# Kernel tuning notes

Hardware: AMD Instinct MI355X
Metric: run time of the kernel (lower is better)

Reference implementation:

```python
import jax, jax.numpy as jnp
import numpy as np

B, L, E, H = 1, 2048, 1024, 16
HW = E // H  # head width = 64
SCALE = HW ** -0.5


def setup_inputs() -> dict:
    key = jax.random.key(0)
    ks = jax.random.split(key, 8)
    x = jax.random.normal(ks[0], (B, L, E), dtype=jnp.float32)
    mask = jax.random.bernoulli(ks[1], 0.9, (B, L))
    mask = mask.at[:, 0].set(True)  # guarantee at least one valid key per batch
    bias = jax.random.normal(ks[2], (B, L, L, H), dtype=jnp.float32)
    # torch nn.Linear stores weight as [out, in]; we keep that convention
    w_proj = jax.random.normal(ks[3], (3 * E, E), dtype=jnp.float32) * (E ** -0.5)
    w_o = jax.random.normal(ks[4], (E, E), dtype=jnp.float32) * (E ** -0.5)
    b_o = jax.random.normal(ks[5], (E,), dtype=jnp.float32) * 0.02
    w_g = jax.random.normal(ks[6], (E, E), dtype=jnp.float32) * (E ** -0.5)
    b_g = jax.random.normal(ks[7], (E,), dtype=jnp.float32) * 0.02
    return {"x": x, "mask": mask, "bias": bias, "w_proj": w_proj,
            "w_o": w_o, "b_o": b_o, "w_g": w_g, "b_g": b_g}


def reference(x, mask, bias, w_proj, w_o, b_o, w_g, b_g):
    # proj -> [B, L, 3E], rearrange '(h c)' with h=H so each head slice holds [q|k|v]
    t = jnp.einsum('ble,fe->blf', x, w_proj)               # [B, L, 3E]
    t = t.reshape(B, L, H, 3 * HW).transpose(0, 2, 1, 3)   # [B, H, L, 3*HW]
    q, k, v = jnp.split(t, 3, axis=-1)                     # each [B, H, L, HW]
    a = jnp.einsum('bhqc,bhkc->bhqk', SCALE * q, k)        # [B, H, L, L]
    a = a + bias.transpose(0, 3, 1, 2)                     # bias: [B,Lq,Lk,H] -> [B,H,Lq,Lk]
    a = jnp.where(mask[:, None, None, :], a, -jnp.inf)
    a = jax.nn.softmax(a, axis=-1)
    y = jnp.einsum('bhqk,bhkc->bqhc', a, v).reshape(B, L, E)
    g = jax.nn.sigmoid(jnp.einsum('ble,fe->blf', x, w_g) + b_g)
    y = g * y
    return jnp.einsum('ble,fe->blf', y, w_o) + b_o
```

## Files before the change

kernel.cpp:

```cpp
#include <hip/hip_runtime.h>
#include <stdint.h>

#define LSEQ 2048
#define EMB  1024
#define NH   16
#define HWID 64
#define SCALEF 0.125f

typedef __attribute__((ext_vector_type(4))) float  f32x4;
typedef __attribute__((ext_vector_type(8))) short  bf16x8;
typedef __attribute__((ext_vector_type(8))) unsigned short u16x8;
typedef __attribute__((ext_vector_type(4))) unsigned short u16x4;

static __device__ __forceinline__ unsigned short f2bf(float f) {
    union { float f; unsigned int u; } v; v.f = f;
    unsigned int r = (v.u + 0x7FFFu + ((v.u >> 16) & 1u)) >> 16;
    return (unsigned short)r;
}
static __device__ __forceinline__ float bf2f(unsigned short h) {
    union { unsigned int u; float f; } v; v.u = ((unsigned int)h) << 16;
    return v.f;
}

static __device__ __forceinline__ void gload_lds16(const void* g, void* l) {
    __builtin_amdgcn_global_load_lds((const __attribute__((address_space(1))) void*)g,
                                     (__attribute__((address_space(3))) void*)l,
                                     16, 0, 0);
}

__global__ __launch_bounds__(256) void convert_kernel(
    const float* __restrict__ x, const float* __restrict__ wp,
    const float* __restrict__ wg, const float* __restrict__ wo,
    unsigned short* __restrict__ xb, unsigned short* __restrict__ wcat,
    unsigned short* __restrict__ wob)
{
    const int NX  = (LSEQ * EMB) / 4;
    const int NWP = (3 * EMB * EMB) / 4;
    const int NWG = (EMB * EMB) / 4;
    const int NWO = (EMB * EMB) / 4;
    const int total = NX + NWP + NWG + NWO;
    for (int i = blockIdx.x * blockDim.x + threadIdx.x; i < total;
         i += gridDim.x * blockDim.x) {
        const float4* src; unsigned short* dst; int j;
        if (i < NX)                  { src = (const float4*)x;  dst = xb;                  j = i; }
        else if (i < NX + NWP)       { src = (const float4*)wp; dst = wcat;                j = i - NX; }
        else if (i < NX + NWP + NWG) { src = (const float4*)wg; dst = wcat + 3 * EMB * EMB; j = i - NX - NWP; }
        else                         { src = (const float4*)wo; dst = wob;                 j = i - NX - NWP - NWG; }
        float4 v = src[j];
        u16x4 o;
        o.x = f2bf(v.x); o.y = f2bf(v.y); o.z = f2bf(v.z); o.w = f2bf(v.w);
        *(u16x4*)(dst + (size_t)j * 4) = o;
    }
}

__global__ void decode_mask_kernel(const unsigned char* __restrict__ mask,
                                   float* __restrict__ mbias)
{
    __shared__ int cnt;
    if (threadIdx.x == 0) cnt = 0;
    __syncthreads();
    int c = 0;
    for (int i = threadIdx.x; i < LSEQ; i += 256) c += (mask[i] != 0);
    atomicAdd(&cnt, c);
    __syncthreads();
    bool isbyte = cnt > LSEQ / 2;
    for (int k = threadIdx.x; k < LSEQ; k += 256) {
        bool v;
        if (isbyte) v = (mask[k] != 0);
        else        v = ((mask[4*k] | mask[4*k+1] | mask[4*k+2] | mask[4*k+3]) != 0);
        mbias[k] = v ? 0.f : -1e30f;
    }
}

#define BM 128
#define BN 128
#define BK 64

__global__ __launch_bounds__(256) void gemm_bt_kernel(
    const unsigned short* __restrict__ A, const unsigned short* __restrict__ B,
    void* __restrict__ Cout, const float* __restrict__ biasN,
    int M, int N, int K, int epi)
{
    __shared__ unsigned short As[BM][BK];
    __shared__ unsigned short Bs[BN][BK];
    const int tid  = threadIdx.x;
    const int lane = tid & 63;
    const int w    = tid >> 6;
    const int wr   = w >> 1, wc = w & 1;
    const int row0 = blockIdx.y * BM;
    const int col0 = blockIdx.x * BN;
    const int lr = lane & 15;
    const int lg = lane >> 4;

    f32x4 acc[4][4];
    const f32x4 zf = {0.f, 0.f, 0.f, 0.f};
#pragma unroll
    for (int m = 0; m < 4; ++m)
#pragma unroll
        for (int n = 0; n < 4; ++n) acc[m][n] = zf;

    const char* Ab = (const char*)(A + (size_t)row0 * K);
    const char* Bb = (const char*)(B + (size_t)col0 * K);
    const int Kb = K * 2;

    for (int kt = 0; kt < K; kt += BK) {
#pragma unroll
        for (int i = 0; i < 4; ++i) {
            int o = (i * 256 + tid) * 16;
            int r = o >> 7, cb = o & 127;
            gload_lds16(Ab + (size_t)r * Kb + kt * 2 + cb, (char*)As + o);
        }
#pragma unroll
        for (int i = 0; i < 4; ++i) {
            int o = (i * 256 + tid) * 16;
            int r = o >> 7, cb = o & 127;
            gload_lds16(Bb + (size_t)r * Kb + kt * 2 + cb, (char*)Bs + o);
        }
        __syncthreads();
#pragma unroll
        for (int kk = 0; kk < 2; ++kk) {
            bf16x8 af[4], bfr[4];
            const int lk = kk * 32 + lg * 8;
#pragma unroll
            for (int m = 0; m < 4; ++m) af[m]  = *(const bf16x8*)&As[wr * 64 + m * 16 + lr][lk];
#pragma unroll
            for (int n = 0; n < 4; ++n) bfr[n] = *(const bf16x8*)&Bs[wc * 64 + n * 16 + lr][lk];
#pragma unroll
            for (int m = 0; m < 4; ++m)
#pragma unroll
                for (int n = 0; n < 4; ++n)
                    acc[m][n] = __builtin_amdgcn_mfma_f32_16x16x32_bf16(af[m], bfr[n], acc[m][n], 0, 0, 0);
        }
        __syncthreads();
    }

#pragma unroll
    for (int m = 0; m < 4; ++m)
#pragma unroll
        for (int n = 0; n < 4; ++n) {
            const int col = col0 + wc * 64 + n * 16 + lr;
#pragma unroll
            for (int r = 0; r < 4; ++r) {
                const int row = row0 + wr * 64 + m * 16 + lg * 4 + r;
                if (epi == 0)
                    ((unsigned short*)Cout)[(size_t)row * N + col] = f2bf(acc[m][n][r]);
                else
                    ((float*)Cout)[(size_t)row * N + col] = acc[m][n][r] + biasN[col];
            }
        }
}

__global__ __launch_bounds__(256) void rearrange_kernel(
    const unsigned short* __restrict__ T, const float* __restrict__ bg,
    unsigned short* __restrict__ Qh, unsigned short* __restrict__ Kh,
    unsigned short* __restrict__ G)
{
    const int l = blockIdx.x;
    const int t = threadIdx.x;
    const unsigned short* trow = T + (size_t)l * 4096;
    {
        const int tt = t & 127;
        const int h  = tt >> 3;
        const int c0 = (tt & 7) * 8;
        const bool isq = (t < 128);
        const int srcoff = h * 192 + (isq ? 0 : 64) + c0;
        u16x8 v = *(const u16x8*)(trow + srcoff);
        if (isq) {
#pragma unroll
            for (int j = 0; j < 8; ++j) v[j] = f2bf(bf2f(v[j]) * SCALEF);
        }
        unsigned short* dst = (isq ? Qh : Kh) + ((size_t)h * LSEQ + l) * HWID + c0;
        *(u16x8*)dst = v;
    }
    {
        const int f0 = t * 4;
        float4 b4 = *(const float4*)(bg + f0);
        u16x4 tv = *(const u16x4*)(trow + 3 * EMB + f0);
        u16x4 o;
        o.x = f2bf(1.f / (1.f + __expf(-(bf2f(tv.x) + b4.x))));
        o.y = f2bf(1.f / (1.f + __expf(-(bf2f(tv.y) + b4.y))));
        o.z = f2bf(1.f / (1.f + __expf(-(bf2f(tv.z) + b4.z))));
        o.w = f2bf(1.f / (1.f + __expf(-(bf2f(tv.w) + b4.w))));
        *(u16x4*)(G + (size_t)l * EMB + f0) = o;
    }
}

__global__ __launch_bounds__(256) void vtrans_kernel(
    const unsigned short* __restrict__ T, unsigned short* __restrict__ VT)
{
    __shared__ unsigned short tile[64][72];
    const int h  = blockIdx.x & 15;
    const int lt = blockIdx.x >> 4;
    const int l0 = lt * 64;
    const int t  = threadIdx.x;
    {
        const int i = t >> 2, c0 = (t & 3) * 16;
        const unsigned short* src = T + (size_t)(l0 + i) * 4096 + h * 192 + 128;
        *(u16x8*)&tile[i][c0]     = *(const u16x8*)(src + c0);
        *(u16x8*)&tile[i][c0 + 8] = *(const u16x8*)(src + c0 + 8);
    }
    __syncthreads();
    {
        const int c = t >> 2, j0 = (t & 3) * 16;
        unsigned short* dst = VT + ((size_t)h * HWID + c) * LSEQ + l0 + j0;
        u16x8 a, b;
#pragma unroll
        for (int j = 0; j < 8; ++j) a[j] = tile[j0 + j][c];
#pragma unroll
        for (int j = 0; j < 8; ++j) b[j] = tile[j0 + 8 + j][c];
        *(u16x8*)dst       = a;
        *(u16x8*)(dst + 8) = b;
    }
}

#define NT 32

__global__ __launch_bounds__(1024) void attn_kernel(
    const unsigned short* __restrict__ Qh, const unsigned short* __restrict__ Kh,
    const unsigned short* __restrict__ VT, const float* __restrict__ bias,
    const float* __restrict__ mbias,
    float* __restrict__ Op, float* __restrict__ Ml)
{
    __shared__ float bias_s[2][16][576];
    __shared__ unsigned short ps[16][16][40];
    __shared__ float mk[1024];

    const int tid  = threadIdx.x;
    const int lane = tid & 63;
    const int w    = tid >> 6;
    const int qsub = blockIdx.x >> 1;
    const int sp   = blockIdx.x & 1;
    const int h    = w;
    const int q0   = qsub * 16;
    const int koff = sp * 1024;
    const int lr   = lane & 15;
    const int lg   = lane >> 4;

    const unsigned short* Qbase = Qh + ((size_t)h * LSEQ + q0) * HWID;
    const bf16x8 qa0 = *(const bf16x8*)(Qbase + lr * HWID + lg * 8);
    const bf16x8 qa1 = *(const bf16x8*)(Qbase + lr * HWID + 32 + lg * 8);

    const unsigned short* Kbase = Kh + ((size_t)h * LSEQ + koff) * HWID;
    const unsigned short* Vbase = VT + (size_t)h * HWID * LSEQ + koff;

    const int li   = tid >> 1;
    const int bq   = li >> 5;
    const int bk   = li & 31;
    const int half = tid & 1;
    const float* bsrc0 = bias +
        ((size_t)(q0 + bq) * LSEQ + (koff + bk)) * NH + half * 8;
    const int bidx = bq * 36 + bk;

    auto loadBias = [&](int t, float4* bv) {
        const float* src = bsrc0 + (size_t)t * 32 * NH;
        bv[0] = *(const float4*)(src);
        bv[1] = *(const float4*)(src + 4);
    };
    auto writeBias = [&](int slot, const float4* bv) {
#pragma unroll
        for (int j = 0; j < 4; ++j) {
            bias_s[slot][half * 8 + j][bidx]     = ((const float*)&bv[0])[j];
            bias_s[slot][half * 8 + 4 + j][bidx] = ((const float*)&bv[1])[j];
        }
    };
    auto loadK = [&](int t, bf16x8 (&kb)[2][2]) {
        const int kgl = t * 32;
#pragma unroll
        for (int t2 = 0; t2 < 2; ++t2) {
            const unsigned short* kp = Kbase + (size_t)(kgl + t2 * 16 + lr) * HWID + lg * 8;
            kb[t2][0] = *(const bf16x8*)kp;
            kb[t2][1] = *(const bf16x8*)(kp + 32);
        }
    };

    bf16x8 ones;
#pragma unroll
    for (int j2 = 0; j2 < 8; ++j2) ones[j2] = (short)0x3F80;

    float mrow[4];
    f32x4 acc[4], lsum;
    const f32x4 zf = {0.f, 0.f, 0.f, 0.f};
#pragma unroll
    for (int r = 0; r < 4; ++r) mrow[r] = -1e30f;
#pragma unroll
    for (int c = 0; c < 4; ++c) acc[c] = zf;
    lsum = zf;

    float4 bv[2];
    bf16x8 kbA[2][2], kbB[2][2];
    loadBias(0, bv);
    loadK(0, kbA);
    mk[tid] = mbias[koff + tid];
    __syncthreads();
    writeBias(0, bv);
    asm volatile("s_waitcnt lgkmcnt(0)" ::: "memory");
    __builtin_amdgcn_s_barrier();

    const unsigned short (*psb)[40] = nullptr; (void)psb;

    auto body = [&](int t, bf16x8 (&kbCur)[2][2], bf16x8 (&kbNxt)[2][2]) {
        const int kgl = t * 32;

        bf16x8 vb[4];
#pragma unroll
        for (int ct = 0; ct < 4; ++ct)
            vb[ct] = *(const bf16x8*)(Vbase + (size_t)(ct * 16 + lr) * LSEQ + kgl + lg * 8);
        asm volatile("" ::: "memory");
        if (t + 1 < NT) loadK(t + 1, kbNxt);
        asm volatile("" ::: "memory");
        if (t + 1 < NT) loadBias(t + 1, bv);
        asm volatile("" ::: "memory");

        f32x4 S[2];
#pragma unroll
        for (int t2 = 0; t2 < 2; ++t2) {
            f32x4 s = zf;
            s = __builtin_amdgcn_mfma_f32_16x16x32_bf16(qa0, kbCur[t2][0], s, 0, 0, 0);
            s = __builtin_amdgcn_mfma_f32_16x16x32_bf16(qa1, kbCur[t2][1], s, 0, 0, 0);
            S[t2] = s;
        }

        const float* bpl = &bias_s[t & 1][w][0];
        const float m0 = mk[kgl + lr];
        const float m1 = mk[kgl + 16 + lr];
        float sc0[4], sc1[4], lm[4];
#pragma unroll
        for (int r = 0; r < 4; ++r) {
            const int qrow = (lg * 4 + r) * 36;
            sc0[r] = S[0][r] + bpl[qrow + lr] + m0;
            sc1[r] = S[1][r] + bpl[qrow + 16 + lr] + m1;
            lm[r] = fmaxf(sc0[r], sc1[r]);
        }
        const float need = fmaxf(fmaxf(lm[0] - mrow[0], lm[1] - mrow[1]),
                                 fmaxf(lm[2] - mrow[2], lm[3] - mrow[3]));
        if (!__all(need <= 8.0f)) {
            float rm[4];
#pragma unroll
            for (int r = 0; r < 4; ++r) rm[r] = lm[r];
#pragma unroll
            for (int off = 1; off < 16; off <<= 1)
#pragma unroll
                for (int r = 0; r < 4; ++r)
                    rm[r] = fmaxf(rm[r], __shfl_xor(rm[r], off, 64));
            float sf[4];
#pragma unroll
            for (int r = 0; r < 4; ++r) {
                const float mn = fmaxf(mrow[r], rm[r]);
                sf[r] = __expf(mrow[r] - mn);
                mrow[r] = mn;
            }
#pragma unroll
            for (int ct = 0; ct < 4; ++ct)
#pragma unroll
                for (int r = 0; r < 4; ++r) acc[ct][r] *= sf[r];
#pragma unroll
            for (int r = 0; r < 4; ++r) lsum[r] *= sf[r];
        }

        float p0[4], p1[4];
#pragma unroll
        for (int r = 0; r < 4; ++r) {
            p0[r] = __expf(sc0[r] - mrow[r]);
            p1[r] = __expf(sc1[r] - mrow[r]);
        }

#pragma unroll
        for (int r = 0; r < 4; ++r) {
            ps[w][lg * 4 + r][lr]      = f2bf(p0[r]);
            ps[w][lg * 4 + r][16 + lr] = f2bf(p1[r]);
        }
        const bf16x8 pa = *(const bf16x8*)&ps[w][lr][lg * 8];

#pragma unroll
        for (int ct = 0; ct < 4; ++ct)
            acc[ct] = __builtin_amdgcn_mfma_f32_16x16x32_bf16(pa, vb[ct], acc[ct], 0, 0, 0);
        lsum = __builtin_amdgcn_mfma_f32_16x16x32_bf16(pa, ones, lsum, 0, 0, 0);

        if (t + 1 < NT) writeBias((t + 1) & 1, bv);
        asm volatile("s_waitcnt lgkmcnt(0)" ::: "memory");
        __builtin_amdgcn_s_barrier();
    };

#pragma unroll 1
    for (int tt = 0; tt < NT; tt += 2) {
        body(tt,     kbA, kbB);
        body(tt + 1, kbB, kbA);
    }

    const size_t rowb = ((size_t)sp * NH + h) * LSEQ;
#pragma unroll
    for (int ct = 0; ct < 4; ++ct)
#pragma unroll
        for (int r = 0; r < 4; ++r) {
            const int q = q0 + lg * 4 + r;
            Op[(rowb + q) * HWID + ct * 16 + lr] = acc[ct][r];
        }
    if (lr == 0) {
#pragma unroll
        for (int r = 0; r < 4; ++r) {
            const int q = q0 + lg * 4 + r;
            Ml[(rowb + q) * 2 + 0] = mrow[r];
            Ml[(rowb + q) * 2 + 1] = lsum[r];
        }
    }
}

__global__ __launch_bounds__(256) void combine_kernel(
    const float* __restrict__ Op, const float* __restrict__ Ml,
    const unsigned short* __restrict__ G, unsigned short* __restrict__ Yb)
{
    const int t   = threadIdx.x;
    const int c   = t & 63;
    const int row = blockIdx.x * 4 + (t >> 6);
    const int h   = row >> 11;
    const int q   = row & (LSEQ - 1);
    const size_t r0 = (size_t)h * LSEQ + q;
    const size_t r1 = ((size_t)NH + h) * LSEQ + q;
    const float m0 = Ml[r0 * 2 + 0], l0 = Ml[r0 * 2 + 1];
    const float m1 = Ml[r1 * 2 + 0], l1 = Ml[r1 * 2 + 1];
    const float mx = fmaxf(m0, m1);
    const float a0 = __expf(m0 - mx), a1 = __expf(m1 - mx);
    const float inv = 1.f / (l0 * a0 + l1 * a1);
    const float o0 = Op[r0 * HWID + c];
    const float o1 = Op[r1 * HWID + c];
    const float y = (o0 * a0 + o1 * a1) * inv;
    const int e = h * HWID + c;
    const float g = bf2f(G[(size_t)q * EMB + e]);
    Yb[(size_t)q * EMB + e] = f2bf(y * g);
}

extern "C" void kernel_launch(void* const* d_in, const int* in_sizes, int n_in,
                              void* d_out, int out_size, void* d_ws, size_t ws_size,
                              hipStream_t stream) {
    const float*         x      = (const float*)d_in[0];
    const unsigned char* mask   = (const unsigned char*)d_in[1];
    const float*         bias   = (const float*)d_in[2];
    const float*         w_proj = (const float*)d_in[3];
    const float*         w_o    = (const float*)d_in[4];
    const float*         b_o    = (const float*)d_in[5];
    const float*         w_g    = (const float*)d_in[6];
    const float*         b_g    = (const float*)d_in[7];
    float* out = (float*)d_out;
    (void)in_sizes; (void)n_in; (void)out_size; (void)ws_size;

    char* p = (char*)d_ws;
    auto alloc = [&](size_t bytes) {
        char* r = p; p += (bytes + 255) & ~(size_t)255; return r;
    };
    unsigned short* xb    = (unsigned short*)alloc((size_t)LSEQ * EMB * 2);
    unsigned short* wcat  = (unsigned short*)alloc((size_t)4 * EMB * EMB * 2);
    unsigned short* wob   = (unsigned short*)alloc((size_t)EMB * EMB * 2);
    unsigned short* T     = (unsigned short*)alloc((size_t)LSEQ * 4096 * 2);
    unsigned short* Qh    = (unsigned short*)alloc((size_t)NH * LSEQ * HWID * 2);
    unsigned short* Kh    = (unsigned short*)alloc((size_t)NH * LSEQ * HWID * 2);
    unsigned short* VT    = (unsigned short*)alloc((size_t)NH * HWID * LSEQ * 2);
    unsigned short* G     = (unsigned short*)alloc((size_t)LSEQ * EMB * 2);
    unsigned short* Yb    = (unsigned short*)alloc((size_t)LSEQ * EMB * 2);
    float*          mb    = (float*)alloc((size_t)LSEQ * 4);
    float*          Op    = (float*)alloc((size_t)2 * NH * LSEQ * HWID * 4);
    float*          Ml    = (float*)alloc((size_t)2 * NH * LSEQ * 2 * 4);

    convert_kernel<<<1024, 256, 0, stream>>>(x, w_proj, w_g, w_o, xb, wcat, wob);
    decode_mask_kernel<<<1, 256, 0, stream>>>(mask, mb);
    gemm_bt_kernel<<<dim3(4096 / BN, LSEQ / BM), 256, 0, stream>>>(
        xb, wcat, (void*)T, nullptr, LSEQ, 4096, EMB, 0);
    rearrange_kernel<<<LSEQ, 256, 0, stream>>>(T, b_g, Qh, Kh, G);
    vtrans_kernel<<<NH * (LSEQ / 64), 256, 0, stream>>>(T, VT);
    attn_kernel<<<256, 1024, 0, stream>>>(Qh, Kh, VT, bias, mb, Op, Ml);
    combine_kernel<<<NH * LSEQ / 4, 256, 0, stream>>>(Op, Ml, G, Yb);
    gemm_bt_kernel<<<dim3(EMB / BN, LSEQ / BM), 256, 0, stream>>>(
        Yb, wob, (void*)out, b_o, LSEQ, EMB, EMB, 1);
}
```

Baseline: 238.0 us.

## Deepen bias prefetch to two tiles ahead with explicit vmcnt waits

Bias loads are now issued two tiles ahead and held in ping-pong register buffers, and K stays one tile ahead. Indices are clamped so the loop no longer needs tail conditionals. Explicit sched_barriers and partial s_waitcnt vmcnt counts replace the compiler's conservative waits, so the MFMA work can start while later global loads are still in flight. In exchange it uses more registers and depends on hand-counted vmcnt values matching the load order the compiler emits. The final iterations also issue redundant clamped loads.

```diff
diff --git a/kernel.cpp b/kernel.cpp
--- a/kernel.cpp
+++ b/kernel.cpp
@@ -252,7 +252,8 @@
     const int bidx = bq * 36 + bk;
 
     auto loadBias = [&](int t, float4* bv) {
-        const float* src = bsrc0 + (size_t)t * 32 * NH;
+        const int tc = (t < NT) ? t : NT - 1;
+        const float* src = bsrc0 + (size_t)tc * 32 * NH;
         bv[0] = *(const float4*)(src);
         bv[1] = *(const float4*)(src + 4);
     };
@@ -264,7 +265,8 @@
         }
     };
     auto loadK = [&](int t, bf16x8 (&kb)[2][2]) {
-        const int kgl = t * 32;
+        const int tc = (t < NT) ? t : NT - 1;
+        const int kgl = tc * 32;
 #pragma unroll
         for (int t2 = 0; t2 < 2; ++t2) {
             const unsigned short* kp = Kbase + (size_t)(kgl + t2 * 16 + lr) * HWID + lg * 8;
@@ -286,31 +288,33 @@
     for (int c = 0; c < 4; ++c) acc[c] = zf;
     lsum = zf;
 
-    float4 bv[2];
+    float4 tmp[2], bvA[2], bvB[2];
     bf16x8 kbA[2][2], kbB[2][2];
-    loadBias(0, bv);
+    loadBias(0, tmp);
+    loadBias(1, bvA);
     loadK(0, kbA);
     mk[tid] = mbias[koff + tid];
     __syncthreads();
-    writeBias(0, bv);
+    writeBias(0, tmp);
     asm volatile("s_waitcnt lgkmcnt(0)" ::: "memory");
     __builtin_amdgcn_s_barrier();
 
-    const unsigned short (*psb)[40] = nullptr; (void)psb;
-
-    auto body = [&](int t, bf16x8 (&kbCur)[2][2], bf16x8 (&kbNxt)[2][2]) {
+    auto body = [&](int t, bf16x8 (&kbCur)[2][2], bf16x8 (&kbNxt)[2][2],
+                    float4 (&bvWr)[2], float4 (&bvRecv)[2]) {
         const int kgl = t * 32;
 
         bf16x8 vb[4];
 #pragma unroll
         for (int ct = 0; ct < 4; ++ct)
             vb[ct] = *(const bf16x8*)(Vbase + (size_t)(ct * 16 + lr) * LSEQ + kgl + lg * 8);
-        asm volatile("" ::: "memory");
-        if (t + 1 < NT) loadK(t + 1, kbNxt);
-        asm volatile("" ::: "memory");
-        if (t + 1 < NT) loadBias(t + 1, bv);
-        asm volatile("" ::: "memory");
-
+        __builtin_amdgcn_sched_barrier(0);
+        loadBias(t + 2, bvRecv);
+        __builtin_amdgcn_sched_barrier(0);
+        loadK(t + 1, kbNxt);
+        __builtin_amdgcn_sched_barrier(0);
+
+        asm volatile("s_waitcnt vmcnt(10)" ::: "memory");
+        __builtin_amdgcn_sched_barrier(0);
         f32x4 S[2];
 #pragma unroll
         for (int t2 = 0; t2 < 2; ++t2) {
@@ -369,22 +373,28 @@
             ps[w][lg * 4 + r][lr]      = f2bf(p0[r]);
             ps[w][lg * 4 + r][16 + lr] = f2bf(p1[r]);
         }
+        asm volatile("s_waitcnt lgkmcnt(0)" ::: "memory");
+        __builtin_amdgcn_sched_barrier(0);
         const bf16x8 pa = *(const bf16x8*)&ps[w][lr][lg * 8];
 
+        asm volatile("s_waitcnt vmcnt(6)" ::: "memory");
+        __builtin_amdgcn_sched_barrier(0);
 #pragma unroll
         for (int ct = 0; ct < 4; ++ct)
             acc[ct] = __builtin_amdgcn_mfma_f32_16x16x32_bf16(pa, vb[ct], acc[ct], 0, 0, 0);
         lsum = __builtin_amdgcn_mfma_f32_16x16x32_bf16(pa, ones, lsum, 0, 0, 0);
-
-        if (t + 1 < NT) writeBias((t + 1) & 1, bv);
+        __builtin_amdgcn_sched_barrier(0);
+
+        writeBias((t + 1) & 1, bvWr);
         asm volatile("s_waitcnt lgkmcnt(0)" ::: "memory");
+        __builtin_amdgcn_sched_barrier(0);
         __builtin_amdgcn_s_barrier();
     };
 
 #pragma unroll 1
     for (int tt = 0; tt < NT; tt += 2) {
-        body(tt,     kbA, kbB);
-        body(tt + 1, kbB, kbA);
+        body(tt,     kbA, kbB, bvA, bvB);
+        body(tt + 1, kbB, kbA, bvB, bvA);
     }
 
     const size_t rowb = ((size_t)sp * NH + h) * LSEQ;
```

Result: slower. 245.5 us (+3.1%).

## Split attention keys four ways and store bias tile in LDS as bf16

Applied to the files above, without the earlier changes.

Increases the key-dimension split from two to four partitions, doubling the attention grid to 512 blocks, and generalizes the combine kernel to merge four partial softmax results. The bias tile staged in shared memory is stored as bf16 instead of fp32, halving its LDS footprint. This aims to improve CU occupancy and latency hiding, at the cost of doubled partial-output traffic and bias rounding error.

```diff
diff --git a/kernel.cpp b/kernel.cpp
--- a/kernel.cpp
+++ b/kernel.cpp
@@ -213,7 +213,8 @@
     }
 }
 
-#define NT 32
+#define SPLITS 4
+#define NT 16
 
 __global__ __launch_bounds__(1024) void attn_kernel(
     const unsigned short* __restrict__ Qh, const unsigned short* __restrict__ Kh,
@@ -221,18 +222,18 @@
     const float* __restrict__ mbias,
     float* __restrict__ Op, float* __restrict__ Ml)
 {
-    __shared__ float bias_s[2][16][576];
+    __shared__ unsigned short bias_s[2][16][576];
     __shared__ unsigned short ps[16][16][40];
-    __shared__ float mk[1024];
+    __shared__ float mk[512];
 
     const int tid  = threadIdx.x;
     const int lane = tid & 63;
     const int w    = tid >> 6;
-    const int qsub = blockIdx.x >> 1;
-    const int sp   = blockIdx.x & 1;
+    const int qsub = blockIdx.x >> 2;
+    const int sp   = blockIdx.x & 3;
     const int h    = w;
     const int q0   = qsub * 16;
-    const int koff = sp * 1024;
+    const int koff = sp * 512;
     const int lr   = lane & 15;
     const int lg   = lane >> 4;
 
@@ -259,8 +260,8 @@
     auto writeBias = [&](int slot, const float4* bv) {
 #pragma unroll
         for (int j = 0; j < 4; ++j) {
-            bias_s[slot][half * 8 + j][bidx]     = ((const float*)&bv[0])[j];
-            bias_s[slot][half * 8 + 4 + j][bidx] = ((const float*)&bv[1])[j];
+            bias_s[slot][half * 8 + j][bidx]     = f2bf(((const float*)&bv[0])[j]);
+            bias_s[slot][half * 8 + 4 + j][bidx] = f2bf(((const float*)&bv[1])[j]);
         }
     };
     auto loadK = [&](int t, bf16x8 (&kb)[2][2]) {
@@ -290,13 +291,11 @@
     bf16x8 kbA[2][2], kbB[2][2];
     loadBias(0, bv);
     loadK(0, kbA);
-    mk[tid] = mbias[koff + tid];
+    if (tid < 512) mk[tid] = mbias[koff + tid];
     __syncthreads();
     writeBias(0, bv);
     asm volatile("s_waitcnt lgkmcnt(0)" ::: "memory");
     __builtin_amdgcn_s_barrier();
-
-    const unsigned short (*psb)[40] = nullptr; (void)psb;
 
     auto body = [&](int t, bf16x8 (&kbCur)[2][2], bf16x8 (&kbNxt)[2][2]) {
         const int kgl = t * 32;
@@ -320,15 +319,15 @@
             S[t2] = s;
         }
 
-        const float* bpl = &bias_s[t & 1][w][0];
+        const unsigned short* bpl = &bias_s[t & 1][w][0];
         const float m0 = mk[kgl + lr];
         const float m1 = mk[kgl + 16 + lr];
         float sc0[4], sc1[4], lm[4];
 #pragma unroll
         for (int r = 0; r < 4; ++r) {
             const int qrow = (lg * 4 + r) * 36;
-            sc0[r] = S[0][r] + bpl[qrow + lr] + m0;
-            sc1[r] = S[1][r] + bpl[qrow + 16 + lr] + m1;
+            sc0[r] = S[0][r] + bf2f(bpl[qrow + lr]) + m0;
+            sc1[r] = S[1][r] + bf2f(bpl[qrow + 16 + lr]) + m1;
             lm[r] = fmaxf(sc0[r], sc1[r]);
         }
         const float need = fmaxf(fmaxf(lm[0] - mrow[0], lm[1] - mrow[1]),
@@ -414,16 +413,25 @@
     const int row = blockIdx.x * 4 + (t >> 6);
     const int h   = row >> 11;
     const int q   = row & (LSEQ - 1);
-    const size_t r0 = (size_t)h * LSEQ + q;
-    const size_t r1 = ((size_t)NH + h) * LSEQ + q;
-    const float m0 = Ml[r0 * 2 + 0], l0 = Ml[r0 * 2 + 1];
-    const float m1 = Ml[r1 * 2 + 0], l1 = Ml[r1 * 2 + 1];
-    const float mx = fmaxf(m0, m1);
-    const float a0 = __expf(m0 - mx), a1 = __expf(m1 - mx);
-    const float inv = 1.f / (l0 * a0 + l1 * a1);
-    const float o0 = Op[r0 * HWID + c];
-    const float o1 = Op[r1 * HWID + c];
-    const float y = (o0 * a0 + o1 * a1) * inv;
+
+    size_t rs[SPLITS];
+    float m[SPLITS], l[SPLITS];
+    float mx = -1e30f;
+#pragma unroll
+    for (int s = 0; s < SPLITS; ++s) {
+        rs[s] = ((size_t)s * NH + h) * LSEQ + q;
+        m[s] = Ml[rs[s] * 2 + 0];
+        l[s] = Ml[rs[s] * 2 + 1];
+        mx = fmaxf(mx, m[s]);
+    }
+    float den = 0.f, y = 0.f;
+#pragma unroll
+    for (int s = 0; s < SPLITS; ++s) {
+        const float a = __expf(m[s] - mx);
+        den += l[s] * a;
+        y   += Op[rs[s] * HWID + c] * a;
+    }
+    y /= den;
     const int e = h * HWID + c;
     const float g = bf2f(G[(size_t)q * EMB + e]);
     Yb[(size_t)q * EMB + e] = f2bf(y * g);
@@ -457,8 +465,8 @@
     unsigned short* G     = (unsigned short*)alloc((size_t)LSEQ * EMB * 2);
     unsigned short* Yb    = (unsigned short*)alloc((size_t)LSEQ * EMB * 2);
     float*          mb    = (float*)alloc((size_t)LSEQ * 4);
-    float*          Op    = (float*)alloc((size_t)2 * NH * LSEQ * HWID * 4);
-    float*          Ml    = (float*)alloc((size_t)2 * NH * LSEQ * 2 * 4);
+    float*          Op    = (float*)alloc((size_t)SPLITS * NH * LSEQ * HWID * 4);
+    float*          Ml    = (float*)alloc((size_t)SPLITS * NH * LSEQ * 2 * 4);
 
     convert_kernel<<<1024, 256, 0, stream>>>(x, w_proj, w_g, w_o, xb, wcat, wob);
     decode_mask_kernel<<<1, 256, 0, stream>>>(mask, mb);
@@ -466,7 +474,7 @@
         xb, wcat, (void*)T, nullptr, LSEQ, 4096, EMB, 0);
     rearrange_kernel<<<LSEQ, 256, 0, stream>>>(T, b_g, Qh, Kh, G);
     vtrans_kernel<<<NH * (LSEQ / 64), 256, 0, stream>>>(T, VT);
-    attn_kernel<<<256, 1024, 0, stream>>>(Qh, Kh, VT, bias, mb, Op, Ml);
+    attn_kernel<<<512, 1024, 0, stream>>>(Qh, Kh, VT, bias, mb, Op, Ml);
     combine_kernel<<<NH * LSEQ / 4, 256, 0, stream>>>(Op, Ml, G, Yb);
     gemm_bt_kernel<<<dim3(EMB / BN, LSEQ / BM), 256, 0, stream>>>(
         Yb, wob, (void*)out, b_o, LSEQ, EMB, EMB, 1);
```

New measurement: 254.6 us. +7.0%, slower.
